# Performance work log

Hardware: AMD Instinct MI355X
Metric: run time of the kernel (lower is better)

## Reference

```python
import jax, jax.numpy as jnp
import numpy as np

NUM_GAUSS = 64
MAX_R = 5.0
ANG_TO_NM = 0.1  # du.ANG_TO_NM_SCALE
L = 4
C_NODE = 256
C_HID = 256
MAX_ATOMS = 100
B = 512      # building blocks
NPB = 32     # atoms per block
K = 20       # max_neighbors
N = B * NPB
E = N * K
GAUSS_COEFF = -0.5 / (MAX_R / (NUM_GAUSS - 1)) ** 2


def setup_inputs() -> dict:
    rng = np.random.default_rng(0)
    # all atoms of a block inside a 2.5A cube -> every pair within MAX_R=5A,
    # so radius_graph capped at K neighbors == K-nearest graph (fixed E).
    pos = (rng.random((B, NPB, 3)) * 2.5).astype(np.float32)
    d = np.linalg.norm(pos[:, :, None, :] - pos[:, None, :, :], axis=-1)  # [B,n,n]
    ii = np.arange(NPB)
    d[:, ii, ii] = np.inf  # loop=False
    nbr = np.argsort(d, axis=-1)[:, :, :K]  # [B,n,K] nearest neighbors
    base = (np.arange(B) * NPB)[:, None, None]
    row = np.broadcast_to(ii[None, :, None], (B, NPB, K)) + base
    col = nbr + base
    edge_index = np.stack([row.reshape(-1), col.reshape(-1)]).astype(np.int64)

    key = jax.random.key(0)
    ks = jax.random.split(key, 8)

    def lin(k, fi, fo):
        return jax.random.normal(k, (L, fi, fo), jnp.float32) / np.sqrt(fi).astype(np.float32)

    d_e_in = 2 * C_NODE + 1 + NUM_GAUSS  # 577
    return {
        'local_coords': jnp.asarray(pos.reshape(N, 3)),
        'atom_types': jax.random.randint(ks[0], (N,), 1, MAX_ATOMS + 1),  # 1..max_atoms
        'edge_index': jnp.asarray(edge_index),
        'batch_bb': jnp.repeat(jnp.arange(B, dtype=jnp.int32), NPB),
        'atom_embed': jax.random.normal(ks[1], (MAX_ATOMS, C_NODE), jnp.float32) * 0.1,
        'offset': jnp.linspace(0.0, MAX_R, NUM_GAUSS, dtype=jnp.float32),
        'We1': lin(ks[2], d_e_in, C_HID), 'be1': jnp.zeros((L, C_HID), jnp.float32),
        'We2': lin(ks[3], C_HID, C_HID), 'be2': jnp.zeros((L, C_HID), jnp.float32),
        'Wn1': lin(ks[4], C_HID + C_NODE, C_HID), 'bn1': jnp.zeros((L, C_HID), jnp.float32),
        'Wn2': lin(ks[5], C_HID, C_NODE), 'bn2': jnp.zeros((L, C_NODE), jnp.float32),
    }


def _forward(local_coords, atom_types, edge_index, batch_bb, atom_embed, offset,
             We1, be1, We2, be2, Wn1, bn1, Wn2, bn2):
    row, col = edge_index[0], edge_index[1]
    h = atom_embed[atom_types - 1]                      # [N, C_NODE]
    # Gaussian smearing of pairwise distances (Angstrom)
    dvec = local_coords[col] - local_coords[row]        # [E, 3]
    dist = jnp.sqrt(jnp.sum(dvec * dvec, axis=-1))      # [E]
    edge_attr = jnp.exp(GAUSS_COEFF * (dist[:, None] - offset[None, :]) ** 2)  # [E, 64]
    coord = local_coords * ANG_TO_NM
    cdiff = coord[row] - coord[col]
    radial = jnp.sum(cdiff * cdiff, axis=-1, keepdims=True)  # [E, 1]
    nblocks = batch_bb.shape[0] // NPB  # static
    for l in range(L):  # small fixed layer count
        e_in = jnp.concatenate([h[row], h[col], radial, edge_attr], axis=-1)  # [E, 577]
        m = jax.nn.relu(e_in @ We1[l] + be1[l])
        m = jax.nn.relu(m @ We2[l] + be2[l])                 # edge_mlp output [E, C_HID]
        agg = jax.ops.segment_sum(m, row, num_segments=N)    # scatter-sum to nodes
        n_in = jnp.concatenate([h, agg], axis=-1)            # [N, C_NODE + C_HID]
        out = jax.nn.relu(n_in @ Wn1[l] + bn1[l]) @ Wn2[l] + bn2[l]
        node_update = h + out                                # residual inside E_GCL
        h = h + node_update                                  # outer residual in forward
    # global_mean_pool over building blocks
    s = jax.ops.segment_sum(h, batch_bb, num_segments=B)
    cnt = jax.ops.segment_sum(jnp.ones((h.shape[0], 1), h.dtype), batch_bb, num_segments=B)
    return s / cnt


def reference(local_coords, atom_types, edge_index, batch_bb, atom_embed, offset,
              We1, be1, We2, be2, Wn1, bn1, Wn2, bn2):
    return _forward(local_coords, atom_types, edge_index, batch_bb, atom_embed, offset,
                    We1, be1, We2, be2, Wn1, bn1, Wn2, bn2)
```

## Files before the change

### kernel.cpp

```cpp
#include <hip/hip_runtime.h>
#include <hip/hip_bf16.h>
#include <stdint.h>

#define NATOMS 16384
#define ETOT   327680
#define NLAYER 4

typedef __hip_bfloat16 bf16;
using bf16x8 = __attribute__((ext_vector_type(8))) short;
using bf16x4 = __attribute__((ext_vector_type(4))) short;
using f32x4  = __attribute__((ext_vector_type(4))) float;

#define LDSF_STRIDE 260

__device__ __forceinline__ float bf2f(short s) {
  union { float f; unsigned u; } x; x.u = ((unsigned)(unsigned short)s) << 16; return x.f;
}
__device__ __forceinline__ short f2bf(float f) {
  bf16 b = __float2bfloat16(f);
  return *(short*)&b;
}

__device__ __forceinline__ void async16(const void* g, void* l) {
  __builtin_amdgcn_global_load_lds(
      (const __attribute__((address_space(1))) unsigned int*)g,
      (__attribute__((address_space(3))) unsigned int*)l, 16, 0, 0);
}

template<int KTOT, int EPI, int MT>
__global__ void __launch_bounds__(256, 2)
gemm_k(const bf16* A, const bf16* A2, const bf16* B,
       bf16* Obf, int ldOut, const float* bias,
       float* Hf, bf16* Hbf)
{
  __shared__ __align__(16) char smem[49152];
  const int tid  = threadIdx.x;
  const int w    = tid >> 6;
  const int lane = tid & 63;
  const int q    = lane >> 4;
  const int t16  = lane & 15;
  const size_t row0 = (size_t)blockIdx.x * MT;
  const int ncol0 = blockIdx.y * 256;
  constexpr int MI = MT / 16;
  constexpr int AI = MT / 32;

  f32x4 acc[MI][4] = {};
  constexpr int NCHUNK = KTOT / 64;
  for (int kc = 0; kc < NCHUNK; ++kc) {
    const int k0 = kc * 64;
    __syncthreads();
    #pragma unroll
    for (int ii = 0; ii < AI; ++ii) {
      int i = w * AI + ii;
      int f = i * 64 + lane;
      int m = f >> 3, s = f & 7;
      int ko = s ^ (m & 7);
      async16(A + (row0 + (size_t)m) * KTOT + (size_t)(k0 + ko * 8), smem + i * 1024);
    }
    #pragma unroll
    for (int ii = 0; ii < 8; ++ii) {
      int i = w * 8 + ii;
      int f = i * 64 + lane;
      int n = f >> 3, s = f & 7;
      int ko = s ^ (n & 7);
      async16(B + (size_t)(ncol0 + n) * KTOT + (size_t)(k0 + ko * 8),
              smem + 16384 + i * 1024);
    }
    __syncthreads();
    #pragma unroll
    for (int ks = 0; ks < 2; ++ks) {
      bf16x8 av[MI]; bf16x8 bv[4];
      const int ko = q + 4 * ks;
      #pragma unroll
      for (int mi = 0; mi < MI; ++mi) {
        int m = 16 * mi + t16;
        int f = m * 8 + (ko ^ (m & 7));
        av[mi] = *(const bf16x8*)(smem + f * 16);
      }
      #pragma unroll
      for (int ni = 0; ni < 4; ++ni) {
        int n = 64 * w + 16 * ni + t16;
        int f = n * 8 + (ko ^ (n & 7));
        bv[ni] = *(const bf16x8*)(smem + 16384 + f * 16);
      }
      #pragma unroll
      for (int mi = 0; mi < MI; ++mi)
        #pragma unroll
        for (int ni = 0; ni < 4; ++ni)
          acc[mi][ni] = __builtin_amdgcn_mfma_f32_16x16x32_bf16(
              av[mi], bv[ni], acc[mi][ni], 0, 0, 0);
    }
  }

  float* lds_f = (float*)smem;
  #pragma unroll
  for (int mi = 0; mi < MI; ++mi) {
    __syncthreads();
    #pragma unroll
    for (int ni = 0; ni < 4; ++ni)
      #pragma unroll
      for (int r = 0; r < 4; ++r)
        lds_f[(4 * q + r) * LDSF_STRIDE + 64 * w + 16 * ni + t16] = acc[mi][ni][r];
    __syncthreads();
    #pragma unroll
    for (int j = 0; j < 2; ++j) {
      int task = tid + 256 * j;
      int rr = task >> 5, cg = task & 31;
      int c0 = cg * 8;
      size_t rg = row0 + 16 * mi + rr;
      f32x4 v0 = *(const f32x4*)(lds_f + rr * LDSF_STRIDE + c0);
      f32x4 v1 = *(const f32x4*)(lds_f + rr * LDSF_STRIDE + c0 + 4);
      float v[8] = {v0[0], v0[1], v0[2], v0[3], v1[0], v1[1], v1[2], v1[3]};
      bf16x8 o;
      #pragma unroll
      for (int k = 0; k < 8; ++k) {
        float vv = v[k];
        if (bias != nullptr && ncol0 == 0) vv += bias[c0 + k];
        o[k] = f2bf(vv);
      }
      *(bf16x8*)(Obf + rg * ldOut + (ncol0 + c0)) = o;
    }
  }
}

#define WINC 40960
#define WINR 57856
#define SCOL 59968
#define SRAD 60288
#define WPITCH 528

__global__ void __launch_bounds__(256, 2)
edge_fused(const bf16* Wgp_l, const bf16* W2p_l, const float* off,
           const float* pos, const int* eidx, const bf16* Prc,
           const float* wrad, const float* be2, bf16* Agg)
{
  __shared__ __align__(16) char smem[60608];
  int*   s_col = (int*)  (smem + SCOL);
  float* s_rad = (float*)(smem + SRAD);

  const int tid  = threadIdx.x;
  const int w    = tid >> 6;
  const int lane = tid & 63;
  const int q    = lane >> 4;
  const int t16  = lane & 15;
  const int blk  = blockIdx.x;
  const int node0  = (blk >> 3) * 32;
  const int rnode0 = blk * 4;
  const int ebase  = blk * 80;

  bf16x8 wgf[4][2];
  #pragma unroll
  for (int fi = 0; fi < 4; ++fi)
    #pragma unroll
    for (int ks = 0; ks < 2; ++ks)
      wgf[fi][ks] = *(const bf16x8*)(Wgp_l + (size_t)(((fi * 2 + ks) * 4 + w) * 512)
                                     + lane * 8);

  {
    int row = tid >> 3, seg = tid & 7;
    const bf16* src = Prc + (size_t)(node0 + row) * 512 + 256 + seg * 32;
    char* dst = smem + WINC + row * WPITCH + seg * 64;
    #pragma unroll
    for (int j = 0; j < 4; ++j)
      *(bf16x8*)(dst + j * 16) = *(const bf16x8*)(src + j * 8);
  }
  if (tid < 128) {
    int row = tid >> 5, seg = tid & 31;
    *(bf16x8*)(smem + WINR + row * WPITCH + seg * 16) =
        *(const bf16x8*)(Prc + (size_t)(rnode0 + row) * 512 + seg * 8);
  }

  if (tid < 80) {
    int e = ebase + tid;
    int rg = rnode0 + tid / 20;
    int cg = eidx[ETOT + e];
    float dx = pos[cg * 3 + 0] - pos[rg * 3 + 0];
    float dy = pos[cg * 3 + 1] - pos[rg * 3 + 1];
    float dz = pos[cg * 3 + 2] - pos[rg * 3 + 2];
    float d2 = dx * dx + dy * dy + dz * dz;
    s_col[tid] = cg & 31;
    s_rad[tid] = 0.01f * d2;
    float d = sqrtf(d2);
    const float GC = -0.5f / ((5.0f / 63.0f) * (5.0f / 63.0f));
    #pragma unroll
    for (int oct = 0; oct < 8; ++oct) {
      bf16x8 v;
      #pragma unroll
      for (int j = 0; j < 8; ++j) {
        float t = d - off[oct * 8 + j];
        v[j] = f2bf(__expf(GC * t * t));
      }
      int f = tid * 8 + (oct ^ (tid & 7));
      *(bf16x8*)(smem + f * 16) = v;
    }
  }
  __syncthreads();

  f32x4 acc1[4][5] = {};
  #pragma unroll
  for (int ks = 0; ks < 2; ++ks) {
    const int ko = q + 4 * ks;
    bf16x8 gv[5];
    #pragma unroll
    for (int ci = 0; ci < 5; ++ci) {
      int e = 16 * ci + t16;
      int f = e * 8 + (ko ^ (e & 7));
      gv[ci] = *(const bf16x8*)(smem + f * 16);
    }
    #pragma unroll
    for (int fi = 0; fi < 4; ++fi)
      #pragma unroll
      for (int ci = 0; ci < 5; ++ci)
        acc1[fi][ci] = __builtin_amdgcn_mfma_f32_16x16x32_bf16(
            wgf[fi][ks], gv[ci], acc1[fi][ci], 0, 0, 0);
  }
  __syncthreads();

  {
    f32x4 tw[4];
    #pragma unroll
    for (int fi = 0; fi < 4; ++fi)
      tw[fi] = *(const f32x4*)(wrad + 64 * w + 16 * fi + 4 * q);
    #pragma unroll
    for (int ci = 0; ci < 5; ++ci) {
      int e = 16 * ci + t16;
      int rl = e / 20;
      int cl = s_col[e];
      float rad = s_rad[e];
      #pragma unroll
      for (int fi = 0; fi < 4; ++fi) {
        int fb = 64 * w + 16 * fi + 4 * q;
        bf16x4 pr = *(const bf16x4*)(smem + WINR + rl * WPITCH + fb * 2);
        bf16x4 pc = *(const bf16x4*)(smem + WINC + cl * WPITCH + fb * 2);
        bf16x4 o;
        #pragma unroll
        for (int r = 0; r < 4; ++r) {
          float val = acc1[fi][ci][r] + rad * tw[fi][r]
                    + bf2f(pr[r]) + bf2f(pc[r]);
          o[r] = f2bf(fmaxf(val, 0.f));
        }
        int u = (16 * w + 4 * fi + q) ^ (e & 14);
        *(bf16x4*)(smem + e * 512 + u * 8) = o;
      }
    }
  }
  __syncthreads();

  f32x4 acc2[5][4] = {};
  #pragma unroll
  for (int kc = 0; kc < 4; ++kc) {
    bf16x8 bv[4][2];
    #pragma unroll
    for (int ni = 0; ni < 4; ++ni)
      #pragma unroll
      for (int ks = 0; ks < 2; ++ks) {
        int frag = kc * 8 + ks * 4 + ni;
        bv[ni][ks] = *(const bf16x8*)(W2p_l + (size_t)((frag * 4 + w) * 512)
                                      + lane * 8);
      }
    #pragma unroll
    for (int ks = 0; ks < 2; ++ks) {
      const int ko = q + 4 * ks;
      bf16x8 av[5];
      #pragma unroll
      for (int mi = 0; mi < 5; ++mi) {
        int e = 16 * mi + t16;
        int ub = (2 * (8 * kc + ko)) ^ (t16 & 14);
        av[mi] = *(const bf16x8*)(smem + e * 512 + ub * 8);
      }
      #pragma unroll
      for (int mi = 0; mi < 5; ++mi)
        #pragma unroll
        for (int ni = 0; ni < 4; ++ni)
          acc2[mi][ni] = __builtin_amdgcn_mfma_f32_16x16x32_bf16(
              av[mi], bv[ni][ks], acc2[mi][ni], 0, 0, 0);
    }
  }

  #pragma unroll
  for (int ni = 0; ni < 4; ++ni) {
    float b = be2[64 * w + 16 * ni + t16];
    float pp[5];
    #pragma unroll
    for (int mi = 0; mi < 5; ++mi) {
      float s = 0.f;
      #pragma unroll
      for (int r = 0; r < 4; ++r) s += fmaxf(acc2[mi][ni][r] + b, 0.f);
      pp[mi] = s;
    }
    #pragma unroll
    for (int nn = 0; nn < 4; ++nn) {
      float s = 0.f;
      #pragma unroll
      for (int mi = 0; mi < 5; ++mi) {
        int g = 4 * mi + q;
        if (g >= 5 * nn && g <= 5 * nn + 4) s += pp[mi];
      }
      s += __shfl_xor(s, 16, 64);
      s += __shfl_xor(s, 32, 64);
      if (q == nn)
        Agg[(size_t)(rnode0 + nn) * 256 + 64 * w + 16 * ni + t16] =
            __float2bfloat16(s);
    }
  }
}

template<bool DO_PRC>
__global__ void __launch_bounds__(256)
node_fused(const bf16* Hbf_in, const bf16* Agg, const bf16* Wn1T_l,
           const bf16* Wn2p_l, const bf16* Wrcp_n,
           const float* bn1, const float* bn2, const float* be1_n,
           float* Hf, bf16* Hbf, bf16* Prc)
{
  __shared__ __align__(16) char smem[73728];
  __shared__ float s_bn1[256];
  __shared__ float s_bn2[256];
  char* T = smem + 40960;

  const int tid  = threadIdx.x;
  const int w    = tid >> 6;
  const int lane = tid & 63;
  const int q    = lane >> 4;
  const int t16  = lane & 15;
  const size_t row0 = (size_t)blockIdx.x * 64;

  s_bn1[tid] = bn1[tid];
  s_bn2[tid] = bn2[tid];

  f32x4 acc[4][4] = {};
  for (int kc = 0; kc < 8; ++kc) {
    const bf16* Asrc = (kc < 4) ? Hbf_in : Agg;
    const int k0e = (kc & 3) * 64;
    __syncthreads();
    #pragma unroll
    for (int ii = 0; ii < 2; ++ii) {
      int i = w * 2 + ii;
      int f = i * 64 + lane;
      int m = f >> 3, s = f & 7;
      int ko = s ^ (m & 7);
      async16(Asrc + (row0 + (size_t)m) * 256 + (size_t)(k0e + ko * 8),
              smem + i * 1024);
    }
    #pragma unroll
    for (int ii = 0; ii < 8; ++ii) {
      int i = w * 8 + ii;
      int f = i * 64 + lane;
      int n = f >> 3, s = f & 7;
      int ko = s ^ (n & 7);
      async16(Wn1T_l + (size_t)n * 512 + (size_t)(kc * 64 + ko * 8),
              smem + 8192 + i * 1024);
    }
    __syncthreads();
    #pragma unroll
    for (int ks = 0; ks < 2; ++ks) {
      bf16x8 av[4]; bf16x8 bv[4];
      const int ko = q + 4 * ks;
      #pragma unroll
      for (int mi = 0; mi < 4; ++mi) {
        int m = 16 * mi + t16;
        int f = m * 8 + (ko ^ (m & 7));
        av[mi] = *(const bf16x8*)(smem + f * 16);
      }
      #pragma unroll
      for (int ni = 0; ni < 4; ++ni) {
        int n = 64 * w + 16 * ni + t16;
        int f = n * 8 + (ko ^ (n & 7));
        bv[ni] = *(const bf16x8*)(smem + 8192 + f * 16);
      }
      #pragma unroll
      for (int mi = 0; mi < 4; ++mi)
        #pragma unroll
        for (int ni = 0; ni < 4; ++ni)
          acc[mi][ni] = __builtin_amdgcn_mfma_f32_16x16x32_bf16(
              av[mi], bv[ni], acc[mi][ni], 0, 0, 0);
    }
  }

  float* lds_f = (float*)smem;
  #pragma unroll
  for (int mi = 0; mi < 4; ++mi) {
    __syncthreads();
    #pragma unroll
    for (int ni = 0; ni < 4; ++ni)
      #pragma unroll
      for (int r = 0; r < 4; ++r)
        lds_f[(4 * q + r) * LDSF_STRIDE + 64 * w + 16 * ni + t16] = acc[mi][ni][r];
    __syncthreads();
    #pragma unroll
    for (int j = 0; j < 2; ++j) {
      int task = tid + 256 * j;
      int rr = task >> 5, cg = task & 31;
      int c0 = cg * 8;
      int rl = 16 * mi + rr;
      f32x4 v0 = *(const f32x4*)(lds_f + rr * LDSF_STRIDE + c0);
      f32x4 v1 = *(const f32x4*)(lds_f + rr * LDSF_STRIDE + c0 + 4);
      float v[8] = {v0[0], v0[1], v0[2], v0[3], v1[0], v1[1], v1[2], v1[3]};
      bf16x8 o;
      #pragma unroll
      for (int k = 0; k < 8; ++k) o[k] = f2bf(fmaxf(v[k] + s_bn1[c0 + k], 0.f));
      int s = (cg & 24) | ((cg & 7) ^ (rl & 7));
      *(bf16x8*)(T + rl * 512 + s * 16) = o;
    }
  }
  __syncthreads();

  f32x4 acc2[4][4] = {};
  #pragma unroll
  for (int kc = 0; kc < 4; ++kc) {
    bf16x8 bv[4][2];
    #pragma unroll
    for (int ni = 0; ni < 4; ++ni)
      #pragma unroll
      for (int ks = 0; ks < 2; ++ks) {
        int frag = kc * 8 + ks * 4 + ni;
        bv[ni][ks] = *(const bf16x8*)(Wn2p_l + (size_t)((frag * 4 + w) * 512)
                                      + lane * 8);
      }
    #pragma unroll
    for (int ks = 0; ks < 2; ++ks) {
      const int ko = q + 4 * ks;
      bf16x8 av[4];
      #pragma unroll
      for (int mi = 0; mi < 4; ++mi) {
        int row = 16 * mi + t16;
        int s = 8 * kc + (ko ^ (t16 & 7));
        av[mi] = *(const bf16x8*)(T + row * 512 + s * 16);
      }
      #pragma unroll
      for (int mi = 0; mi < 4; ++mi)
        #pragma unroll
        for (int ni = 0; ni < 4; ++ni)
          acc2[mi][ni] = __builtin_amdgcn_mfma_f32_16x16x32_bf16(
              av[mi], bv[ni][ks], acc2[mi][ni], 0, 0, 0);
    }
  }

  #pragma unroll
  for (int mi = 0; mi < 4; ++mi) {
    __syncthreads();
    #pragma unroll
    for (int ni = 0; ni < 4; ++ni)
      #pragma unroll
      for (int r = 0; r < 4; ++r)
        lds_f[(4 * q + r) * LDSF_STRIDE + 64 * w + 16 * ni + t16] = acc2[mi][ni][r];
    __syncthreads();
    #pragma unroll
    for (int j = 0; j < 2; ++j) {
      int task = tid + 256 * j;
      int rr = task >> 5, cg = task & 31;
      int c0 = cg * 8;
      int rl = 16 * mi + rr;
      size_t rg = row0 + rl;
      f32x4 v0 = *(const f32x4*)(lds_f + rr * LDSF_STRIDE + c0);
      f32x4 v1 = *(const f32x4*)(lds_f + rr * LDSF_STRIDE + c0 + 4);
      float v[8] = {v0[0], v0[1], v0[2], v0[3], v1[0], v1[1], v1[2], v1[3]};
      f32x4 h0 = *(const f32x4*)(Hf + rg * 256 + c0);
      f32x4 h1 = *(const f32x4*)(Hf + rg * 256 + c0 + 4);
      float hh[8] = {h0[0], h0[1], h0[2], h0[3], h1[0], h1[1], h1[2], h1[3]};
      bf16x8 o; f32x4 n0, n1;
      #pragma unroll
      for (int k = 0; k < 8; ++k) {
        float hn = 2.f * hh[k] + v[k] + s_bn2[c0 + k];
        o[k] = f2bf(hn);
        if (k < 4) n0[k] = hn; else n1[k - 4] = hn;
      }
      *(f32x4*)(Hf + rg * 256 + c0)     = n0;
      *(f32x4*)(Hf + rg * 256 + c0 + 4) = n1;
      *(bf16x8*)(Hbf + rg * 256 + c0) = o;
      int s = (cg & 24) | ((cg & 7) ^ (rl & 7));
      *(bf16x8*)(T + rl * 512 + s * 16) = o;
    }
  }

  if constexpr (DO_PRC) {
    __syncthreads();
    #pragma unroll
    for (int nh = 0; nh < 2; ++nh) {
      f32x4 acc3[4][4] = {};
      #pragma unroll
      for (int kc = 0; kc < 4; ++kc) {
        bf16x8 bv[4][2];
        #pragma unroll
        for (int ni = 0; ni < 4; ++ni)
          #pragma unroll
          for (int ks = 0; ks < 2; ++ks) {
            int frag = kc * 8 + ks * 4 + ni;
            bv[ni][ks] = *(const bf16x8*)(Wrcp_n + (size_t)nh * 65536 +
                                          (size_t)((frag * 4 + w) * 512) + lane * 8);
          }
        #pragma unroll
        for (int ks = 0; ks < 2; ++ks) {
          const int ko = q + 4 * ks;
          bf16x8 av[4];
          #pragma unroll
          for (int mi = 0; mi < 4; ++mi) {
            int row = 16 * mi + t16;
            int s = 8 * kc + (ko ^ (t16 & 7));
            av[mi] = *(const bf16x8*)(T + row * 512 + s * 16);
          }
          #pragma unroll
          for (int mi = 0; mi < 4; ++mi)
            #pragma unroll
            for (int ni = 0; ni < 4; ++ni)
              acc3[mi][ni] = __builtin_amdgcn_mfma_f32_16x16x32_bf16(
                  av[mi], bv[ni][ks], acc3[mi][ni], 0, 0, 0);
        }
      }
      #pragma unroll
      for (int mi = 0; mi < 4; ++mi) {
        __syncthreads();
        #pragma unroll
        for (int ni = 0; ni < 4; ++ni)
          #pragma unroll
          for (int r = 0; r < 4; ++r)
            lds_f[(4 * q + r) * LDSF_STRIDE + 64 * w + 16 * ni + t16] = acc3[mi][ni][r];
        __syncthreads();
        #pragma unroll
        for (int j = 0; j < 2; ++j) {
          int task = tid + 256 * j;
          int rr = task >> 5, cg = task & 31;
          int c0 = cg * 8;
          size_t rg = row0 + 16 * mi + rr;
          f32x4 v0 = *(const f32x4*)(lds_f + rr * LDSF_STRIDE + c0);
          f32x4 v1 = *(const f32x4*)(lds_f + rr * LDSF_STRIDE + c0 + 4);
          float v[8] = {v0[0], v0[1], v0[2], v0[3], v1[0], v1[1], v1[2], v1[3]};
          bf16x8 o;
          #pragma unroll
          for (int k = 0; k < 8; ++k) {
            float vv = v[k];
            if (nh == 0) vv += be1_n[c0 + k];
            o[k] = f2bf(vv);
          }
          *(bf16x8*)(Prc + rg * 512 + nh * 256 + c0) = o;
        }
      }
    }
  }
}

__global__ void wrct_kernel(const float* We1, bf16* WrcT) {
  int idx = blockIdx.x * 256 + threadIdx.x;
  int k = idx & 255, np = (idx >> 8) & 511;
  float v = (np < 256)
      ? We1[((size_t)k) * 256 + np]
      : We1[((size_t)256 + k) * 256 + (np - 256)];
  WrcT[idx] = __float2bfloat16(v);
}
__global__ void wgp_kernel(const float* We1, bf16* Wgp) {
  int idx = blockIdx.x * 256 + threadIdx.x;
  int i = idx & 16383, l = idx >> 14;
  int j = i & 7, lane = (i >> 3) & 63, w = (i >> 9) & 3, fr = i >> 11;
  int fi = fr >> 1, ks = fr & 1;
  int t16 = lane & 15, q = lane >> 4;
  int g = (q + 4 * ks) * 8 + j;
  int feat = 64 * w + 16 * fi + t16;
  Wgp[idx] = __float2bfloat16(We1[((size_t)l * 577 + 513 + g) * 256 + feat]);
}
__global__ void w2p_kernel(const float* W, bf16* Wp) {
  int idx = blockIdx.x * 256 + threadIdx.x;
  int i = idx & 65535, l = idx >> 16;
  int j = i & 7, lane = (i >> 3) & 63, w = (i >> 9) & 3, fr = i >> 11;
  int ni = fr & 3, ks = (fr >> 2) & 1, kc = fr >> 3;
  int t16 = lane & 15, q = lane >> 4;
  int k = kc * 64 + (q + 4 * ks) * 8 + j;
  int n = 64 * w + 16 * ni + t16;
  Wp[idx] = __float2bfloat16(W[((size_t)l * 256 + k) * 256 + n]);
}
__global__ void wrcp_kernel(const float* We1, bf16* Wrcp) {
  int idx = blockIdx.x * 256 + threadIdx.x;
  int i = idx & 65535, nh = (idx >> 16) & 1, l = idx >> 17;
  int j = i & 7, lane = (i >> 3) & 63, w = (i >> 9) & 3, fr = i >> 11;
  int ni = fr & 3, ks = (fr >> 2) & 1, kc = fr >> 3;
  int t16 = lane & 15, q = lane >> 4;
  int k = kc * 64 + (q + 4 * ks) * 8 + j;
  int n = 64 * w + 16 * ni + t16;
  Wrcp[idx] = __float2bfloat16(We1[((size_t)l * 577 + nh * 256 + k) * 256 + n]);
}
__global__ void wrad_kernel(const float* We1, float* wrad) {
  int idx = blockIdx.x * 256 + threadIdx.x;
  int n = idx & 255, l = idx >> 8;
  wrad[idx] = We1[((size_t)l * 577 + 512) * 256 + n];
}
__global__ void trans_kernel(const float* src, bf16* dst, int R, int C) {
  int idx = blockIdx.x * 256 + threadIdx.x;
  int k = idx % R, rest = idx / R;
  int n = rest % C, l = rest / C;
  dst[idx] = __float2bfloat16(src[((size_t)l * R + k) * C + n]);
}

__global__ void h0_kernel(const int* types, const float* emb, float* h, bf16* hbf) {
  int i = blockIdx.x, c = threadIdx.x;
  float v = emb[(size_t)(types[i] - 1) * 256 + c];
  h[(size_t)i * 256 + c] = v;
  hbf[(size_t)i * 256 + c] = __float2bfloat16(v);
}

__global__ void pool_kernel(const float* h, float* out) {
  int b = blockIdx.x, c = threadIdx.x;
  float s = 0.f;
  #pragma unroll
  for (int j = 0; j < 32; ++j) s += h[((size_t)b * 32 + j) * 256 + c];
  out[(size_t)b * 256 + c] = s * (1.0f / 32.0f);
}

extern "C" void kernel_launch(void* const* d_in, const int* in_sizes, int n_in,
                              void* d_out, int out_size, void* d_ws, size_t ws_size,
                              hipStream_t stream) {
  const float* pos   = (const float*)d_in[0];
  const int*   atype = (const int*)  d_in[1];
  const int*   eidx  = (const int*)  d_in[2];
  const float* emb   = (const float*)d_in[4];
  const float* off   = (const float*)d_in[5];
  const float* We1   = (const float*)d_in[6];
  const float* be1   = (const float*)d_in[7];
  const float* We2   = (const float*)d_in[8];
  const float* be2   = (const float*)d_in[9];
  const float* Wn1   = (const float*)d_in[10];
  const float* bn1   = (const float*)d_in[11];
  const float* Wn2   = (const float*)d_in[12];
  const float* bn2   = (const float*)d_in[13];
  float* out = (float*)d_out;

  size_t o = 0;
  auto carve = [&](size_t bytes) {
    void* p = (char*)d_ws + o;
    o += (bytes + 255) & ~(size_t)255;
    return p;
  };
  float* h     = (float*)carve((size_t)NATOMS * 256 * 4);
  bf16*  hbf   = (bf16*) carve((size_t)NATOMS * 256 * 2);
  bf16*  Prc   = (bf16*) carve((size_t)NATOMS * 512 * 2);
  bf16*  aggbf = (bf16*) carve((size_t)NATOMS * 256 * 2);
  bf16*  WrcT  = (bf16*) carve((size_t)512 * 256 * 2);
  bf16*  Wgp   = (bf16*) carve((size_t)NLAYER * 16384 * 2);
  bf16*  W2p   = (bf16*) carve((size_t)NLAYER * 65536 * 2);
  bf16*  Wn1T  = (bf16*) carve((size_t)NLAYER * 256 * 512 * 2);
  bf16*  Wn2p  = (bf16*) carve((size_t)NLAYER * 65536 * 2);
  bf16*  Wrcp  = (bf16*) carve((size_t)NLAYER * 2 * 65536 * 2);
  float* wradp = (float*)carve((size_t)NLAYER * 256 * 4);

  wrct_kernel<<< 512, 256, 0, stream>>>(We1, WrcT);
  wgp_kernel <<< 256, 256, 0, stream>>>(We1, Wgp);
  w2p_kernel <<<1024, 256, 0, stream>>>(We2, W2p);
  w2p_kernel <<<1024, 256, 0, stream>>>(Wn2, Wn2p);
  wrcp_kernel<<<2048, 256, 0, stream>>>(We1, Wrcp);
  wrad_kernel<<<   4, 256, 0, stream>>>(We1, wradp);
  trans_kernel<<<2048, 256, 0, stream>>>(Wn1, Wn1T, 512, 256);
  h0_kernel  <<<NATOMS, 256, 0, stream>>>(atype, emb, h, hbf);

  gemm_k<256, 0, 64><<<dim3(256, 2), 256, 0, stream>>>(
      hbf, nullptr, WrcT, Prc, 512, be1, nullptr, nullptr);

  for (int l = 0; l < NLAYER; ++l) {
    edge_fused<<<ETOT / 80, 256, 0, stream>>>(
        Wgp + (size_t)l * 16384, W2p + (size_t)l * 65536, off, pos,
        eidx, Prc, wradp + l * 256, be2 + l * 256, aggbf);
    if (l < NLAYER - 1) {
      node_fused<true><<<256, 256, 0, stream>>>(
          hbf, aggbf, Wn1T + (size_t)l * 131072, Wn2p + (size_t)l * 65536,
          Wrcp + (size_t)(l + 1) * 131072, bn1 + l * 256, bn2 + l * 256,
          be1 + (l + 1) * 256, h, hbf, Prc);
    } else {
      node_fused<false><<<256, 256, 0, stream>>>(
          hbf, aggbf, Wn1T + (size_t)l * 131072, Wn2p + (size_t)l * 65536,
          nullptr, bn1 + l * 256, bn2 + l * 256, nullptr, h, hbf, nullptr);
    }
  }

  pool_kernel<<<512, 256, 0, stream>>>(h, out);
}
```

Baseline: 607.0 us.

## Halve node_fused row tile to 32 and read Wn1 fragments from global

The node kernel now handles 32 rows per block instead of 64, launching 512 blocks rather than 256, and asks for two blocks per CU. The first GEMM is rewritten to preload the whole [32x512] activation tile into LDS once. Pre-packed Wn1 MFMA fragments (from a new wn1p_kernel) are read directly from global memory, with weights as the A operand and nodes as B. This removes the per-k-chunk LDS staging and syncs and the LDS round-trip in the first epilogue. The aim is better occupancy and fill on a GPU with many CUs, at the cost of reloading weights from global or L2 twice as often in total.

```diff
diff --git a/kernel.cpp b/kernel.cpp
--- a/kernel.cpp
+++ b/kernel.cpp
@@ -306,105 +306,81 @@
 }
 
 template<bool DO_PRC>
-__global__ void __launch_bounds__(256)
-node_fused(const bf16* Hbf_in, const bf16* Agg, const bf16* Wn1T_l,
+__global__ void __launch_bounds__(256, 2)
+node_fused(const bf16* Hbf_in, const bf16* Agg, const bf16* Wn1p_l,
            const bf16* Wn2p_l, const bf16* Wrcp_n,
            const float* bn1, const float* bn2, const float* be1_n,
            float* Hf, bf16* Hbf, bf16* Prc)
 {
-  __shared__ __align__(16) char smem[73728];
+  __shared__ __align__(16) char smem[49152];
   __shared__ float s_bn1[256];
   __shared__ float s_bn2[256];
-  char* T = smem + 40960;
+  char* T = smem + 32768;
+  float* lds_f = (float*)smem;
 
   const int tid  = threadIdx.x;
   const int w    = tid >> 6;
   const int lane = tid & 63;
   const int q    = lane >> 4;
   const int t16  = lane & 15;
-  const size_t row0 = (size_t)blockIdx.x * 64;
-
+  const size_t row0 = (size_t)blockIdx.x * 32;
+
+  #pragma unroll
+  for (int ii = 0; ii < 8; ++ii) {
+    int i = w * 8 + ii;
+    int ko = (lane & 56) | ((lane & 7) ^ (i & 7));
+    const bf16* srcp = ((lane < 32) ? Hbf_in : Agg)
+                     + (row0 + (size_t)i) * 256 + ((ko * 8) & 255);
+    async16(srcp, smem + i * 1024);
+  }
   s_bn1[tid] = bn1[tid];
   s_bn2[tid] = bn2[tid];
-
-  f32x4 acc[4][4] = {};
+  __syncthreads();
+
+  f32x4 acc1[4][2] = {};
   for (int kc = 0; kc < 8; ++kc) {
-    const bf16* Asrc = (kc < 4) ? Hbf_in : Agg;
-    const int k0e = (kc & 3) * 64;
-    __syncthreads();
-    #pragma unroll
-    for (int ii = 0; ii < 2; ++ii) {
-      int i = w * 2 + ii;
-      int f = i * 64 + lane;
-      int m = f >> 3, s = f & 7;
-      int ko = s ^ (m & 7);
-      async16(Asrc + (row0 + (size_t)m) * 256 + (size_t)(k0e + ko * 8),
-              smem + i * 1024);
-    }
-    #pragma unroll
-    for (int ii = 0; ii < 8; ++ii) {
-      int i = w * 8 + ii;
-      int f = i * 64 + lane;
-      int n = f >> 3, s = f & 7;
-      int ko = s ^ (n & 7);
-      async16(Wn1T_l + (size_t)n * 512 + (size_t)(kc * 64 + ko * 8),
-              smem + 8192 + i * 1024);
-    }
-    __syncthreads();
     #pragma unroll
     for (int ks = 0; ks < 2; ++ks) {
-      bf16x8 av[4]; bf16x8 bv[4];
-      const int ko = q + 4 * ks;
-      #pragma unroll
-      for (int mi = 0; mi < 4; ++mi) {
-        int m = 16 * mi + t16;
-        int f = m * 8 + (ko ^ (m & 7));
-        av[mi] = *(const bf16x8*)(smem + f * 16);
-      }
-      #pragma unroll
-      for (int ni = 0; ni < 4; ++ni) {
-        int n = 64 * w + 16 * ni + t16;
-        int f = n * 8 + (ko ^ (n & 7));
-        bv[ni] = *(const bf16x8*)(smem + 8192 + f * 16);
-      }
-      #pragma unroll
-      for (int mi = 0; mi < 4; ++mi)
-        #pragma unroll
-        for (int ni = 0; ni < 4; ++ni)
-          acc[mi][ni] = __builtin_amdgcn_mfma_f32_16x16x32_bf16(
-              av[mi], bv[ni], acc[mi][ni], 0, 0, 0);
-    }
-  }
-
-  float* lds_f = (float*)smem;
-  #pragma unroll
-  for (int mi = 0; mi < 4; ++mi) {
-    __syncthreads();
-    #pragma unroll
-    for (int ni = 0; ni < 4; ++ni)
+      const int ko = kc * 8 + q + 4 * ks;
+      bf16x8 af[4];
+      #pragma unroll
+      for (int fi = 0; fi < 4; ++fi)
+        af[fi] = *(const bf16x8*)(Wn1p_l +
+                   (size_t)((fi * 16 + kc * 2 + ks) * 4 + w) * 512 + lane * 8);
+      bf16x8 bv[2];
+      #pragma unroll
+      for (int ci = 0; ci < 2; ++ci) {
+        int node = 16 * ci + t16;
+        int sl = (ko & 56) | ((ko & 7) ^ (node & 7));
+        bv[ci] = *(const bf16x8*)(smem + node * 1024 + sl * 16);
+      }
+      #pragma unroll
+      for (int fi = 0; fi < 4; ++fi)
+        #pragma unroll
+        for (int ci = 0; ci < 2; ++ci)
+          acc1[fi][ci] = __builtin_amdgcn_mfma_f32_16x16x32_bf16(
+              af[fi], bv[ci], acc1[fi][ci], 0, 0, 0);
+    }
+  }
+
+  #pragma unroll
+  for (int ci = 0; ci < 2; ++ci) {
+    int node = 16 * ci + t16;
+    #pragma unroll
+    for (int fi = 0; fi < 4; ++fi) {
+      int fb = 64 * w + 16 * fi + 4 * q;
+      f32x4 tb = *(const f32x4*)(s_bn1 + fb);
+      bf16x4 o;
       #pragma unroll
       for (int r = 0; r < 4; ++r)
-        lds_f[(4 * q + r) * LDSF_STRIDE + 64 * w + 16 * ni + t16] = acc[mi][ni][r];
-    __syncthreads();
-    #pragma unroll
-    for (int j = 0; j < 2; ++j) {
-      int task = tid + 256 * j;
-      int rr = task >> 5, cg = task & 31;
-      int c0 = cg * 8;
-      int rl = 16 * mi + rr;
-      f32x4 v0 = *(const f32x4*)(lds_f + rr * LDSF_STRIDE + c0);
-      f32x4 v1 = *(const f32x4*)(lds_f + rr * LDSF_STRIDE + c0 + 4);
-      float v[8] = {v0[0], v0[1], v0[2], v0[3], v1[0], v1[1], v1[2], v1[3]};
-      bf16x8 o;
-      #pragma unroll
-      for (int k = 0; k < 8; ++k) o[k] = f2bf(fmaxf(v[k] + s_bn1[c0 + k], 0.f));
-      int s = (cg & 24) | ((cg & 7) ^ (rl & 7));
-      *(bf16x8*)(T + rl * 512 + s * 16) = o;
+        o[r] = f2bf(fmaxf(acc1[fi][ci][r] + tb[r], 0.f));
+      int u = (16 * w + 4 * fi + q) ^ (node & 14);
+      *(bf16x4*)(T + node * 512 + u * 8) = o;
     }
   }
   __syncthreads();
 
-  f32x4 acc2[4][4] = {};
+  f32x4 acc2[2][4] = {};
   #pragma unroll
   for (int kc = 0; kc < 4; ++kc) {
     bf16x8 bv[4][2];
@@ -419,15 +395,15 @@
     #pragma unroll
     for (int ks = 0; ks < 2; ++ks) {
       const int ko = q + 4 * ks;
-      bf16x8 av[4];
-      #pragma unroll
-      for (int mi = 0; mi < 4; ++mi) {
+      bf16x8 av[2];
+      #pragma unroll
+      for (int mi = 0; mi < 2; ++mi) {
         int row = 16 * mi + t16;
-        int s = 8 * kc + (ko ^ (t16 & 7));
-        av[mi] = *(const bf16x8*)(T + row * 512 + s * 16);
-      }
-      #pragma unroll
-      for (int mi = 0; mi < 4; ++mi)
+        int ub = (2 * (8 * kc + ko)) ^ (t16 & 14);
+        av[mi] = *(const bf16x8*)(T + row * 512 + ub * 8);
+      }
+      #pragma unroll
+      for (int mi = 0; mi < 2; ++mi)
         #pragma unroll
         for (int ni = 0; ni < 4; ++ni)
           acc2[mi][ni] = __builtin_amdgcn_mfma_f32_16x16x32_bf16(
@@ -436,7 +412,7 @@
   }
 
   #pragma unroll
-  for (int mi = 0; mi < 4; ++mi) {
+  for (int mi = 0; mi < 2; ++mi) {
     __syncthreads();
     #pragma unroll
     for (int ni = 0; ni < 4; ++ni)
@@ -467,7 +443,7 @@
       *(f32x4*)(Hf + rg * 256 + c0)     = n0;
       *(f32x4*)(Hf + rg * 256 + c0 + 4) = n1;
       *(bf16x8*)(Hbf + rg * 256 + c0) = o;
-      int s = (cg & 24) | ((cg & 7) ^ (rl & 7));
+      int s = cg ^ ((rl >> 1) & 7);
       *(bf16x8*)(T + rl * 512 + s * 16) = o;
     }
   }
@@ -476,7 +452,7 @@
     __syncthreads();
     #pragma unroll
     for (int nh = 0; nh < 2; ++nh) {
-      f32x4 acc3[4][4] = {};
+      f32x4 acc3[2][4] = {};
       #pragma unroll
       for (int kc = 0; kc < 4; ++kc) {
         bf16x8 bv[4][2];
@@ -491,15 +467,15 @@
         #pragma unroll
         for (int ks = 0; ks < 2; ++ks) {
           const int ko = q + 4 * ks;
-          bf16x8 av[4];
+          bf16x8 av[2];
           #pragma unroll
-          for (int mi = 0; mi < 4; ++mi) {
+          for (int mi = 0; mi < 2; ++mi) {
             int row = 16 * mi + t16;
-            int s = 8 * kc + (ko ^ (t16 & 7));
-            av[mi] = *(const bf16x8*)(T + row * 512 + s * 16);
+            int ub = (2 * (8 * kc + ko)) ^ (t16 & 14);
+            av[mi] = *(const bf16x8*)(T + row * 512 + ub * 8);
           }
           #pragma unroll
-          for (int mi = 0; mi < 4; ++mi)
+          for (int mi = 0; mi < 2; ++mi)
             #pragma unroll
             for (int ni = 0; ni < 4; ++ni)
               acc3[mi][ni] = __builtin_amdgcn_mfma_f32_16x16x32_bf16(
@@ -507,7 +483,7 @@
         }
       }
       #pragma unroll
-      for (int mi = 0; mi < 4; ++mi) {
+      for (int mi = 0; mi < 2; ++mi) {
         __syncthreads();
         #pragma unroll
         for (int ni = 0; ni < 4; ++ni)
@@ -576,16 +552,20 @@
   int n = 64 * w + 16 * ni + t16;
   Wrcp[idx] = __float2bfloat16(We1[((size_t)l * 577 + nh * 256 + k) * 256 + n]);
 }
+__global__ void wn1p_kernel(const float* Wn1, bf16* Wn1p) {
+  int idx = blockIdx.x * 256 + threadIdx.x;
+  int i = idx & 131071, l = idx >> 17;
+  int j = i & 7, lane = (i >> 3) & 63, w = (i >> 9) & 3, fr = i >> 11;
+  int fi = fr >> 4, kc = (fr & 15) >> 1, ks = fr & 1;
+  int t16 = lane & 15, q = lane >> 4;
+  int feat = 64 * w + 16 * fi + t16;
+  int k = kc * 64 + (q + 4 * ks) * 8 + j;
+  Wn1p[idx] = __float2bfloat16(Wn1[((size_t)l * 512 + k) * 256 + feat]);
+}
 __global__ void wrad_kernel(const float* We1, float* wrad) {
   int idx = blockIdx.x * 256 + threadIdx.x;
   int n = idx & 255, l = idx >> 8;
   wrad[idx] = We1[((size_t)l * 577 + 512) * 256 + n];
-}
-__global__ void trans_kernel(const float* src, bf16* dst, int R, int C) {
-  int idx = blockIdx.x * 256 + threadIdx.x;
-  int k = idx % R, rest = idx / R;
-  int n = rest % C, l = rest / C;
-  dst[idx] = __float2bfloat16(src[((size_t)l * R + k) * C + n]);
 }
 
 __global__ void h0_kernel(const int* types, const float* emb, float* h, bf16* hbf) {
@@ -634,7 +614,7 @@
   bf16*  WrcT  = (bf16*) carve((size_t)512 * 256 * 2);
   bf16*  Wgp   = (bf16*) carve((size_t)NLAYER * 16384 * 2);
   bf16*  W2p   = (bf16*) carve((size_t)NLAYER * 65536 * 2);
-  bf16*  Wn1T  = (bf16*) carve((size_t)NLAYER * 256 * 512 * 2);
+  bf16*  Wn1p  = (bf16*) carve((size_t)NLAYER * 131072 * 2);
   bf16*  Wn2p  = (bf16*) carve((size_t)NLAYER * 65536 * 2);
   bf16*  Wrcp  = (bf16*) carve((size_t)NLAYER * 2 * 65536 * 2);
   float* wradp = (float*)carve((size_t)NLAYER * 256 * 4);
@@ -644,8 +624,8 @@
   w2p_kernel <<<1024, 256, 0, stream>>>(We2, W2p);
   w2p_kernel <<<1024, 256, 0, stream>>>(Wn2, Wn2p);
   wrcp_kernel<<<2048, 256, 0, stream>>>(We1, Wrcp);
+  wn1p_kernel<<<2048, 256, 0, stream>>>(Wn1, Wn1p);
   wrad_kernel<<<   4, 256, 0, stream>>>(We1, wradp);
-  trans_kernel<<<2048, 256, 0, stream>>>(Wn1, Wn1T, 512, 256);
   h0_kernel  <<<NATOMS, 256, 0, stream>>>(atype, emb, h, hbf);
 
   gemm_k<256, 0, 64><<<dim3(256, 2), 256, 0, stream>>>(
@@ -656,13 +636,13 @@
         Wgp + (size_t)l * 16384, W2p + (size_t)l * 65536, off, pos,
         eidx, Prc, wradp + l * 256, be2 + l * 256, aggbf);
     if (l < NLAYER - 1) {
-      node_fused<true><<<256, 256, 0, stream>>>(
-          hbf, aggbf, Wn1T + (size_t)l * 131072, Wn2p + (size_t)l * 65536,
+      node_fused<true><<<512, 256, 0, stream>>>(
+          hbf, aggbf, Wn1p + (size_t)l * 131072, Wn2p + (size_t)l * 65536,
           Wrcp + (size_t)(l + 1) * 131072, bn1 + l * 256, bn2 + l * 256,
           be1 + (l + 1) * 256, h, hbf, Prc);
     } else {
-      node_fused<false><<<256, 256, 0, stream>>>(
-          hbf, aggbf, Wn1T + (size_t)l * 131072, Wn2p + (size_t)l * 65536,
+      node_fused<false><<<512, 256, 0, stream>>>(
+          hbf, aggbf, Wn1p + (size_t)l * 131072, Wn2p + (size_t)l * 65536,
           nullptr, bn1 + l * 256, bn2 + l * 256, nullptr, h, hbf, nullptr);
     }
   }
```

Result: faster. 581.4 us (median of 2 runs) (-4.2%).
